# Kernel optimization log

Measured on AMD Instinct MI355X. Metric: run time of the kernel, lower is better.

The kernel has to match this reference:

```python
import jax, jax.numpy as jnp
import numpy as np

B, T, C, H = 2, 2048, 1024, 16
DH = C // H  # head_size = 64
EPS = 1e-5


def layernorm_axis1(x, gamma, beta):
    # Faithful to the torch code: mean/var over dim 1 (TIME axis), unbiased var.
    mean = jnp.mean(x, axis=1, keepdims=True)
    var = jnp.var(x, axis=1, ddof=1, keepdims=True)
    xhat = (x - mean) / jnp.sqrt(var + EPS)
    return gamma * xhat + beta


def setup_inputs() -> dict:
    key = jax.random.key(0)
    ks = jax.random.split(key, 16)
    s_in = 1.0 / np.sqrt(C)
    s_cat = 1.0 / np.sqrt(H * DH)
    s_ff = 1.0 / np.sqrt(4 * C)
    return {
        "x": jax.random.normal(ks[0], (B, T, C), dtype=jnp.float32),
        # per-head Q/K/V projections (no bias), stacked: [H, C, DH]
        "Wq": jax.random.uniform(ks[1], (H, C, DH), jnp.float32, -s_in, s_in),
        "Wk": jax.random.uniform(ks[2], (H, C, DH), jnp.float32, -s_in, s_in),
        "Wv": jax.random.uniform(ks[3], (H, C, DH), jnp.float32, -s_in, s_in),
        # attention output projection [H*DH, C] + bias
        "Wo": jax.random.uniform(ks[4], (H * DH, C), jnp.float32, -s_cat, s_cat),
        "bo": jax.random.uniform(ks[5], (C,), jnp.float32, -s_cat, s_cat),
        # FFN
        "W1": jax.random.uniform(ks[6], (C, 4 * C), jnp.float32, -s_in, s_in),
        "b1": jax.random.uniform(ks[7], (4 * C,), jnp.float32, -s_in, s_in),
        "W2": jax.random.uniform(ks[8], (4 * C, C), jnp.float32, -s_ff, s_ff),
        "b2": jax.random.uniform(ks[9], (C,), jnp.float32, -s_ff, s_ff),
        # LayerNorm affine params (plain tensors in the original)
        "gamma1": jnp.ones((C,), jnp.float32),
        "beta1": jnp.zeros((C,), jnp.float32),
        "gamma2": jnp.ones((C,), jnp.float32),
        "beta2": jnp.zeros((C,), jnp.float32),
    }


def reference(x, Wq, Wk, Wv, Wo, bo, W1, b1, W2, b2, gamma1, beta1, gamma2, beta2):
    # --- pre-LN attention sublayer ---
    x1 = layernorm_axis1(x, gamma1, beta1)                     # [B,T,C]
    q = jnp.einsum("btc,hcd->bhtd", x1, Wq)                    # [B,H,T,DH]
    k = jnp.einsum("btc,hcd->bhtd", x1, Wk)
    v = jnp.einsum("btc,hcd->bhtd", x1, Wv)
    # NOTE: scaled by full embedding dim C (not head_size) — faithful to source.
    scores = jnp.einsum("bhtd,bhsd->bhts", q, k) * (C ** -0.5)  # [B,H,T,T]
    causal = jnp.tril(jnp.ones((T, T), dtype=bool))
    scores = jnp.where(causal, scores, -jnp.inf)
    wei = jax.nn.softmax(scores, axis=-1)
    attn = jnp.einsum("bhts,bhsd->bhtd", wei, v)               # [B,H,T,DH]
    attn = attn.transpose(0, 2, 1, 3).reshape(B, T, H * DH)    # concat heads
    x = x + attn @ Wo + bo
    # --- pre-LN FFN sublayer ---
    x2 = layernorm_axis1(x, gamma2, beta2)
    h = jax.nn.relu(x2 @ W1 + b1)
    x = x + h @ W2 + b2
    return x
```

## Files before the change

### kernel.cpp

```cpp
#include <hip/hip_runtime.h>
#include <math.h>


#define TDIM 2048
#define BDIM 2
#define CDIM 1024
#define HDIM 16
#define DHE  64
#define QKVS 3072
#define NT   32
#define LNEPS 1e-5f
#define SC2  0.0450842200278f

typedef float f32x4 __attribute__((ext_vector_type(4)));
typedef __bf16 bf16x8 __attribute__((ext_vector_type(8)));
typedef __bf16 bf16x4 __attribute__((ext_vector_type(4)));

__device__ __forceinline__ void gld_lds16(const __bf16* g, __bf16* l) {
  __builtin_amdgcn_global_load_lds(
      (const __attribute__((address_space(1))) void*)g,
      (__attribute__((address_space(3))) void*)l, 16, 0, 0);
}

__global__ __launch_bounds__(256) void ln_stats(const float* __restrict__ x,
                                                float* __restrict__ sumv,
                                                float* __restrict__ sqv) {
  int c = blockIdx.x * 256 + threadIdx.x;
  int b = blockIdx.y;
  int t0 = blockIdx.z * (TDIM / 16);
  const float* xp = x + ((size_t)b * TDIM + t0) * CDIM + c;
  float s = 0.f, q = 0.f;
  for (int t = 0; t < TDIM / 16; ++t) {
    float v = xp[(size_t)t * CDIM];
    s += v;
    q += v * v;
  }
  atomicAdd(&sumv[b * CDIM + c], s);
  atomicAdd(&sqv[b * CDIM + c], q);
}

__global__ __launch_bounds__(256) void ln_apply(const float* __restrict__ x,
    const float* __restrict__ sumv, const float* __restrict__ sqv,
    const float* __restrict__ gamma, const float* __restrict__ beta,
    __bf16* __restrict__ y) {
  size_t i = (size_t)blockIdx.x * 256 + threadIdx.x;
  int c = (int)(i & (CDIM - 1));
  int b = (int)(i >> 21);
  float mean = sumv[b * CDIM + c] * (1.f / TDIM);
  float var = (sqv[b * CDIM + c] - mean * mean * (float)TDIM) * (1.f / (TDIM - 1));
  float rstd = rsqrtf(var + LNEPS);
  y[i] = (__bf16)(gamma[c] * (x[i] - mean) * rstd + beta[c]);
}

__global__ __launch_bounds__(256) void pack_all(
    const float* __restrict__ Wq, const float* __restrict__ Wk,
    const float* __restrict__ Wv, const float* __restrict__ Wo,
    const float* __restrict__ W1, const float* __restrict__ W2,
    __bf16* __restrict__ Wqkvb, __bf16* __restrict__ Wob,
    __bf16* __restrict__ W1b, __bf16* __restrict__ W2b) {
  __shared__ float tile[32][33];
  int t = blockIdx.x;
  int tx = threadIdx.x & 31, ty = threadIdx.x >> 5;
  if (t < 3072) {
    int mat = t >> 10, rem = t & 1023;
    int h = rem >> 6, rr = rem & 63;
    int c0 = (rr & 31) * 32, d0 = (rr >> 5) * 32;
    const float* W = (mat == 0) ? Wq : (mat == 1) ? Wk : Wv;
#pragma unroll
    for (int i = 0; i < 4; ++i)
      tile[ty + i * 8][tx] = W[((size_t)h * CDIM + c0 + ty + i * 8) * DHE + d0 + tx];
    __syncthreads();
#pragma unroll
    for (int i = 0; i < 4; ++i) {
      int n = mat * 1024 + h * 64 + d0 + ty + i * 8;
      Wqkvb[(size_t)n * CDIM + c0 + tx] = (__bf16)tile[tx][ty + i * 8];
    }
  } else {
    const float* in; __bf16* outp; int Cc, R, l;
    if (t < 4096)      { in = Wo; outp = Wob; R = 1024; Cc = 1024; l = t - 3072; }
    else if (t < 8192) { in = W1; outp = W1b; R = 1024; Cc = 4096; l = t - 4096; }
    else               { in = W2; outp = W2b; R = 4096; Cc = 1024; l = t - 8192; }
    int ncx = Cc >> 5;
    int c0 = (l % ncx) * 32, r0 = (l / ncx) * 32;
#pragma unroll
    for (int i = 0; i < 4; ++i)
      tile[ty + i * 8][tx] = in[(size_t)(r0 + ty + i * 8) * Cc + c0 + tx];
    __syncthreads();
#pragma unroll
    for (int i = 0; i < 4; ++i)
      outp[(size_t)(c0 + ty + i * 8) * R + r0 + tx] = (__bf16)tile[tx][ty + i * 8];
  }
}

__global__ __launch_bounds__(256) void transp_v(const __bf16* __restrict__ qkv,
    __bf16* __restrict__ vtb) {
  __shared__ __bf16 tile[32][33];
  int bh = blockIdx.y >> 1, d0 = (blockIdx.y & 1) * 32;
  int b = bh >> 4, h = bh & 15;
  int t0 = blockIdx.x * 32;
  int tx = threadIdx.x & 31, ty = threadIdx.x >> 5;
#pragma unroll
  for (int i = 0; i < 4; ++i)
    tile[ty + i * 8][tx] = qkv[((size_t)b * TDIM + t0 + ty + i * 8) * QKVS + 2048 + h * DHE + d0 + tx];
  __syncthreads();
#pragma unroll
  for (int i = 0; i < 4; ++i)
    vtb[((size_t)bh * 64 + d0 + ty + i * 8) * TDIM + t0 + tx] = tile[tx][ty + i * 8];
}

template<bool BIAS, bool RELU, bool OUTBF>
__global__ __launch_bounds__(512, 2) void gemm256(
    const __bf16* __restrict__ Ag, const __bf16* __restrict__ Bg,
    const float* __restrict__ bias, void* __restrict__ Cm, void* __restrict__ Cm2,
    int M, int N, int K, int ld, int gnx) {
  __shared__ __align__(16) char lds[131072];
  int tid = threadIdx.x;
  int lane = tid & 63, wid = tid >> 6;
  int wm = wid >> 2, wn = wid & 3;
  int l15 = lane & 15, hi = lane >> 4;

  size_t koff = (size_t)blockIdx.y * K;
  Ag += koff; Bg += koff;
  void* Cuse = blockIdx.y ? Cm2 : Cm;

  int nwg = gridDim.x;
  int q = nwg >> 3, r = nwg & 7;
  int xcd = blockIdx.x & 7, pos = blockIdx.x >> 3;
  int wgid = (xcd < r ? xcd * (q + 1) : r * (q + 1) + (xcd - r) * q) + pos;
  int m0 = (wgid / gnx) * 256, n0 = (wgid % gnx) * 256;

  int srow = tid >> 2;
  int skcol = ((tid & 3) ^ ((tid >> 3) & 3)) << 3;
  const int acS = ((hi ^ ((l15 >> 1) & 3)) << 4);

  f32x4 acc[8][4];
#pragma unroll
  for (int i = 0; i < 8; ++i)
#pragma unroll
    for (int j = 0; j < 4; ++j) acc[i][j] = (f32x4){0.f, 0.f, 0.f, 0.f};

  auto stageM = [&](const __bf16* __restrict__ G, int grow0, int k0, char* dst) {
#pragma unroll
    for (int c = 0; c < 2; ++c)
      gld_lds16(G + (size_t)(grow0 + c * 128 + srow) * ld + k0 + skcol,
                (__bf16*)(dst + c * 8192) + (size_t)tid * 8);
  };
  auto stageT = [&](int t) {
    char* dst = lds + (size_t)(t & 3) * 32768;
    stageM(Ag, m0, t << 5, dst);
    stageM(Bg, n0, t << 5, dst + 16384);
  };

  int KT = K >> 5;
  stageT(0); stageT(1); stageT(2);
  asm volatile("s_waitcnt vmcnt(8)" ::: "memory");
  __builtin_amdgcn_s_barrier();

  bf16x8 a[8], b[4];
  for (int t = 0; t < KT; ++t) {
    if (t + 3 < KT) stageT(t + 3);
    const char* buf = lds + (size_t)(t & 3) * 32768;
#pragma unroll
    for (int i = 0; i < 8; ++i)
      a[i] = *(const bf16x8*)(buf + (wm * 128 + i * 16 + l15) * 64 + acS);
#pragma unroll
    for (int j = 0; j < 4; ++j)
      b[j] = *(const bf16x8*)(buf + 16384 + (wn * 64 + j * 16 + l15) * 64 + acS);
    __builtin_amdgcn_s_setprio(1);
#pragma unroll
    for (int i = 0; i < 8; ++i)
#pragma unroll
      for (int j = 0; j < 4; ++j)
        acc[i][j] = __builtin_amdgcn_mfma_f32_16x16x32_bf16(a[i], b[j], acc[i][j], 0, 0, 0);
    __builtin_amdgcn_s_setprio(0);
    if (t + 1 < KT) {
      asm volatile("" ::: "memory");
      if (t + 3 < KT)      asm volatile("s_waitcnt vmcnt(8)" ::: "memory");
      else if (t + 2 < KT) asm volatile("s_waitcnt vmcnt(4)" ::: "memory");
      else                 asm volatile("s_waitcnt vmcnt(0)" ::: "memory");
      __builtin_amdgcn_s_barrier();
    }
  }

#pragma unroll
  for (int fm = 0; fm < 8; ++fm) {
    int row = m0 + wm * 128 + fm * 16 + hi * 4;
#pragma unroll
    for (int fn = 0; fn < 4; ++fn) {
      int col = n0 + wn * 64 + fn * 16 + l15;
#pragma unroll
      for (int j = 0; j < 4; ++j) {
        float v = acc[fm][fn][j];
        size_t off = (size_t)(row + j) * N + col;
        if (BIAS) v += bias[col];
        if (RELU) v = fmaxf(v, 0.f);
        if (OUTBF) ((__bf16*)Cuse)[off] = (__bf16)v;
        else       ((float*)Cuse)[off] = v;
      }
    }
  }
}

__global__ __launch_bounds__(256) void splitk_reduce(const float* __restrict__ p0,
    const float* __restrict__ p1, const float* __restrict__ bias,
    const float* __restrict__ res, float* __restrict__ out) {
  size_t i = ((size_t)blockIdx.x * 256 + threadIdx.x) * 4;
  int c = (int)(i & (CDIM - 1));
  float4 a = *(const float4*)(p0 + i);
  float4 b = *(const float4*)(p1 + i);
  float4 r = *(const float4*)(res + i);
  float4 bb = *(const float4*)(bias + c);
  float4 v;
  v.x = a.x + b.x + r.x + bb.x;
  v.y = a.y + b.y + r.y + bb.y;
  v.z = a.z + b.z + r.z + bb.z;
  v.w = a.w + b.w + r.w + bb.w;
  *(float4*)(out + i) = v;
}

__global__ __launch_bounds__(512, 4) void attn_mfma(const __bf16* __restrict__ qkv,
    const __bf16* __restrict__ vt, __bf16* __restrict__ o) {
  __shared__ __align__(16) char smem[55296];
  __bf16 (*Ks)[64][72] = (__bf16 (*)[64][72])(smem);
  __bf16 (*Vs)[64][72] = (__bf16 (*)[64][72])(smem + 18432);
  __bf16 (*Ps)[16][72] = (__bf16 (*)[16][72])(smem + 36864);
  float (*Os)[64]      = (float (*)[64])(smem);
  float* ms = (float*)(smem + 16384);
  float* ls = (float*)(smem + 16640);

  int bh = blockIdx.y;
  int b = bh >> 4, h = bh & 15;
  int bxA = blockIdx.x;
  int bxB = NT - 1 - bxA;
  int tid = threadIdx.x;
  int lane = tid & 63, w = tid >> 6;
  int wq = w & 3;
  int g = w >> 2;
  int l15 = lane & 15, hi = lane >> 4;
  int hi4 = hi * 4;
  size_t bT = (size_t)b * TDIM;

  bf16x8 onesb;
#pragma unroll
  for (int i = 0; i < 8; ++i) onesb[i] = (l15 == 0) ? (__bf16)1.0f : (__bf16)0.0f;

  bf16x8 qfA[2], qfB[2];
  {
    const __bf16* qp = qkv + (bT + bxA * 64 + wq * 16 + l15) * QKVS + h * DHE;
    qfA[0] = *(const bf16x8*)(qp + hi * 8);
    qfA[1] = *(const bf16x8*)(qp + 32 + hi * 8);
    qp = qkv + (bT + bxB * 64 + wq * 16 + l15) * QKVS + h * DHE;
    qfB[0] = *(const bf16x8*)(qp + hi * 8);
    qfB[1] = *(const bf16x8*)(qp + 32 + hi * 8);
  }

  float mA = -INFINITY, mB = -INFINITY;
  f32x4 lA = (f32x4){0.f, 0.f, 0.f, 0.f};
  f32x4 lB = (f32x4){0.f, 0.f, 0.f, 0.f};
  f32x4 oA[4], oB[4];
#pragma unroll
  for (int n = 0; n < 4; ++n) {
    oA[n] = (f32x4){0.f, 0.f, 0.f, 0.f};
    oB[n] = (f32x4){0.f, 0.f, 0.f, 0.f};
  }

  int g_tid = tid & 255;
  int r0 = g_tid >> 3, c8 = (g_tid & 7) * 8;

  auto process = [&](const bf16x8* qf, float& m_i, f32x4& l_acc, f32x4* oacc,
                     int bx, int t2) {
    f32x4 sacc[4];
#pragma unroll
    for (int n = 0; n < 4; ++n) sacc[n] = (f32x4){0.f, 0.f, 0.f, 0.f};
    __builtin_amdgcn_s_setprio(1);
#pragma unroll
    for (int n = 0; n < 4; ++n)
#pragma unroll
      for (int kk = 0; kk < 2; ++kk) {
        bf16x8 kf = *(const bf16x8*)&Ks[g][n * 16 + l15][kk * 32 + hi * 8];
        sacc[n] = __builtin_amdgcn_mfma_f32_16x16x32_bf16(kf, qf[kk], sacc[n], 0, 0, 0);
      }
    __builtin_amdgcn_s_setprio(0);

    int myq = wq * 16 + l15;
    if (t2 == bx) {
#pragma unroll
      for (int n = 0; n < 4; ++n)
#pragma unroll
        for (int j = 0; j < 4; ++j)
          if (n * 16 + hi4 + j > myq) sacc[n][j] = -INFINITY;
    }

    float mx = sacc[0][0];
#pragma unroll
    for (int n = 0; n < 4; ++n) {
      float a0 = fmaxf(sacc[n][0], sacc[n][1]);
      float a1 = fmaxf(sacc[n][2], sacc[n][3]);
      mx = fmaxf(mx, fmaxf(a0, a1));
    }
    mx = fmaxf(mx, __shfl_xor(mx, 16));
    mx = fmaxf(mx, __shfl_xor(mx, 32));
    mx *= SC2;

    if (!__all(mx - m_i <= 8.0f)) {
      float nm = fmaxf(m_i, mx);
      float al = exp2f(m_i - nm);
      m_i = nm;
#pragma unroll
      for (int r = 0; r < 4; ++r) {
        float ao = __shfl(al, hi4 + r);
        l_acc[r] *= ao;
#pragma unroll
        for (int n = 0; n < 4; ++n) oacc[n][r] *= ao;
      }
    }

    float negm = -m_i;
#pragma unroll
    for (int n = 0; n < 4; ++n) {
      bf16x4 pv;
#pragma unroll
      for (int j = 0; j < 4; ++j)
        pv[j] = (__bf16)exp2f(fmaf(sacc[n][j], SC2, negm));
      *(bf16x4*)&Ps[w][l15][n * 16 + hi4] = pv;
    }

    bf16x8 pa0 = *(const bf16x8*)&Ps[w][l15][hi * 8];
    bf16x8 pa1 = *(const bf16x8*)&Ps[w][l15][32 + hi * 8];
    __builtin_amdgcn_s_setprio(1);
#pragma unroll
    for (int n = 0; n < 4; ++n) {
      bf16x8 vf0 = *(const bf16x8*)&Vs[g][n * 16 + l15][hi * 8];
      bf16x8 vf1 = *(const bf16x8*)&Vs[g][n * 16 + l15][32 + hi * 8];
      oacc[n] = __builtin_amdgcn_mfma_f32_16x16x32_bf16(pa0, vf0, oacc[n], 0, 0, 0);
      oacc[n] = __builtin_amdgcn_mfma_f32_16x16x32_bf16(pa1, vf1, oacc[n], 0, 0, 0);
    }
    l_acc = __builtin_amdgcn_mfma_f32_16x16x32_bf16(pa0, onesb, l_acc, 0, 0, 0);
    l_acc = __builtin_amdgcn_mfma_f32_16x16x32_bf16(pa1, onesb, l_acc, 0, 0, 0);
    __builtin_amdgcn_s_setprio(0);
  };

  for (int j = 0; j <= bxB / 2; ++j) {
    int t2 = 2 * j + g;
    bool have = (t2 <= bxB);
    __syncthreads();
    if (have) {
#pragma unroll
      for (int rr = 0; rr < 2; ++rr) {
        int row = rr * 32 + r0;
        *(bf16x8*)&Ks[g][row][c8] =
            *(const bf16x8*)(qkv + (bT + t2 * 64 + row) * QKVS + 1024 + h * DHE + c8);
        *(bf16x8*)&Vs[g][row][c8] =
            *(const bf16x8*)(vt + ((size_t)bh * 64 + row) * TDIM + t2 * 64 + c8);
      }
    }
    __syncthreads();
    if (t2 <= bxA) process(qfA, mA, lA, oA, bxA, t2);
    if (have)      process(qfB, mB, lB, oB, bxB, t2);
  }

  auto merge = [&](int bx, float m_i, const f32x4& l_acc, f32x4* oacc) {
    float m_o[4], l_o[4];
#pragma unroll
    for (int r = 0; r < 4; ++r) {
      m_o[r] = __shfl(m_i, hi4 + r);
      l_o[r] = __shfl(l_acc[r], lane & 48);
    }
    __syncthreads();
    if (g == 1) {
#pragma unroll
      for (int r = 0; r < 4; ++r) {
        int lrow = wq * 16 + hi4 + r;
        if (l15 == 0) { ms[lrow] = m_o[r]; ls[lrow] = l_o[r]; }
#pragma unroll
        for (int n = 0; n < 4; ++n)
          Os[lrow][n * 16 + l15] = oacc[n][r];
      }
    }
    __syncthreads();
    if (g == 0) {
#pragma unroll
      for (int r = 0; r < 4; ++r) {
        int lrow = wq * 16 + hi4 + r;
        float m1 = ms[lrow], l1 = ls[lrow];
        float mm = fmaxf(m_o[r], m1);
        float e0 = exp2f(m_o[r] - mm), e1 = exp2f(m1 - mm);
        float inv = 1.f / (l_o[r] * e0 + l1 * e1);
        size_t row = bT + bx * 64 + lrow;
#pragma unroll
        for (int n = 0; n < 4; ++n) {
          float v = (oacc[n][r] * e0 + Os[lrow][n * 16 + l15] * e1) * inv;
          o[row * CDIM + h * DHE + n * 16 + l15] = (__bf16)v;
        }
      }
    }
  };
  merge(bxA, mA, lA, oA);
  merge(bxB, mB, lB, oB);
}

extern "C" void kernel_launch(void* const* d_in, const int* in_sizes, int n_in,
                              void* d_out, int out_size, void* d_ws, size_t ws_size,
                              hipStream_t stream) {
  (void)in_sizes; (void)n_in; (void)out_size; (void)ws_size;
  const float* x   = (const float*)d_in[0];
  const float* Wq  = (const float*)d_in[1];
  const float* Wk  = (const float*)d_in[2];
  const float* Wv  = (const float*)d_in[3];
  const float* Wo  = (const float*)d_in[4];
  const float* bo  = (const float*)d_in[5];
  const float* W1  = (const float*)d_in[6];
  const float* b1  = (const float*)d_in[7];
  const float* W2  = (const float*)d_in[8];
  const float* b2  = (const float*)d_in[9];
  const float* g1  = (const float*)d_in[10];
  const float* be1 = (const float*)d_in[11];
  const float* g2  = (const float*)d_in[12];
  const float* be2 = (const float*)d_in[13];
  float* out = (float*)d_out;

  char* wsb = (char*)d_ws;
  const size_t MB = 1024 * 1024;
  __bf16* Wqkvb = (__bf16*)(wsb + 0);
  __bf16* Wob   = (__bf16*)(wsb + 6  * MB);
  __bf16* W1b   = (__bf16*)(wsb + 8  * MB);
  __bf16* W2b   = (__bf16*)(wsb + 16 * MB);
  __bf16* qkvb  = (__bf16*)(wsb + 24 * MB);
  __bf16* hb    = (__bf16*)(wsb + 24 * MB);
  __bf16* vtb   = (__bf16*)(wsb + 48 * MB);
  __bf16* x1b   = (__bf16*)(wsb + 56 * MB);
  __bf16* attnb = (__bf16*)(wsb + 56 * MB);
  float*  xmid  = (float*) (wsb + 64 * MB);
  __bf16* x2b   = (__bf16*)(wsb + 80 * MB);
  float*  stats = (float*) (wsb + 88 * MB);
  float*  q0    = (float*) (wsb + 24 * MB);
  float*  q1    = (float*) (wsb + 40 * MB);
  float*  p0    = (float*) (wsb + 0);
  float*  p1    = (float*) (wsb + 48 * MB);
  float* sum1 = stats,        *sq1 = stats + 2048;
  float* sum2 = stats + 4096, *sq2 = stats + 6144;

  hipMemsetAsync(stats, 0, 4 * 2048 * sizeof(float), stream);

  pack_all<<<dim3(12288), 256, 0, stream>>>(Wq, Wk, Wv, Wo, W1, W2,
                                            Wqkvb, Wob, W1b, W2b);

  ln_stats<<<dim3(CDIM / 256, BDIM, 16), 256, 0, stream>>>(x, sum1, sq1);
  ln_apply<<<dim3((BDIM * TDIM * CDIM) / 256), 256, 0, stream>>>(x, sum1, sq1, g1, be1, x1b);

  gemm256<false, false, true><<<dim3(192, 1), 512, 0, stream>>>(
      x1b, Wqkvb, nullptr, qkvb, qkvb, 4096, 3072, 1024, 1024, 12);

  transp_v<<<dim3(TDIM / 32, 64), 256, 0, stream>>>(qkvb, vtb);

  attn_mfma<<<dim3(NT / 2, BDIM * HDIM), 512, 0, stream>>>(qkvb, vtb, attnb);

  gemm256<false, false, false><<<dim3(64, 2), 512, 0, stream>>>(
      attnb, Wob, nullptr, q0, q1, 4096, 1024, 512, 1024, 4);
  splitk_reduce<<<dim3(4096), 256, 0, stream>>>(q0, q1, bo, x, xmid);

  ln_stats<<<dim3(CDIM / 256, BDIM, 16), 256, 0, stream>>>(xmid, sum2, sq2);
  ln_apply<<<dim3((BDIM * TDIM * CDIM) / 256), 256, 0, stream>>>(xmid, sum2, sq2, g2, be2, x2b);

  gemm256<true, true, true><<<dim3(256, 1), 512, 0, stream>>>(
      x2b, W1b, b1, hb, hb, 4096, 4096, 1024, 1024, 16);

  gemm256<false, false, false><<<dim3(64, 2), 512, 0, stream>>>(
      hb, W2b, nullptr, p0, p1, 4096, 1024, 2048, 4096, 4);
  splitk_reduce<<<dim3(4096), 256, 0, stream>>>(p0, p1, b2, xmid, out);
}
```

Before: 270.1 us.

## Split GEMM k-step into two half-phases interleaving loads with MFMA

Restructures the GEMM main loop so each k-step runs as two phases. Each phase loads half of the A fragments and issues half of the global-to-LDS staging (A tile first, then B tile), separated by barriers and sched_barriers. This is meant to spread memory issue across compute, ping-pong style, and to halve the A fragment registers. In exchange it adds extra workgroup barriers per iteration, which can stall waves.

```diff
diff --git a/kernel.cpp b/kernel.cpp
--- a/kernel.cpp
+++ b/kernel.cpp
@@ -145,41 +145,60 @@
       gld_lds16(G + (size_t)(grow0 + c * 128 + srow) * ld + k0 + skcol,
                 (__bf16*)(dst + c * 8192) + (size_t)tid * 8);
   };
-  auto stageT = [&](int t) {
-    char* dst = lds + (size_t)(t & 3) * 32768;
+
+  int KT = K >> 5;
+#pragma unroll
+  for (int t = 0; t < 3; ++t) {
+    char* dst = lds + (size_t)t * 32768;
     stageM(Ag, m0, t << 5, dst);
     stageM(Bg, n0, t << 5, dst + 16384);
-  };
-
-  int KT = K >> 5;
-  stageT(0); stageT(1); stageT(2);
+  }
   asm volatile("s_waitcnt vmcnt(8)" ::: "memory");
   __builtin_amdgcn_s_barrier();
 
-  bf16x8 a[8], b[4];
+  bf16x8 a[4], b[4];
   for (int t = 0; t < KT; ++t) {
-    if (t + 3 < KT) stageT(t + 3);
     const char* buf = lds + (size_t)(t & 3) * 32768;
-#pragma unroll
-    for (int i = 0; i < 8; ++i)
+    char* bufn = lds + (size_t)((t + 3) & 3) * 32768;
+    bool st = (t + 3 < KT);
+    int k3 = (t + 3) << 5;
+
+#pragma unroll
+    for (int i = 0; i < 4; ++i)
       a[i] = *(const bf16x8*)(buf + (wm * 128 + i * 16 + l15) * 64 + acS);
 #pragma unroll
     for (int j = 0; j < 4; ++j)
       b[j] = *(const bf16x8*)(buf + 16384 + (wn * 64 + j * 16 + l15) * 64 + acS);
+    if (st) stageM(Ag, m0, k3, bufn);
+    __builtin_amdgcn_s_barrier();
+    __builtin_amdgcn_sched_barrier(0);
     __builtin_amdgcn_s_setprio(1);
 #pragma unroll
-    for (int i = 0; i < 8; ++i)
+    for (int i = 0; i < 4; ++i)
 #pragma unroll
       for (int j = 0; j < 4; ++j)
         acc[i][j] = __builtin_amdgcn_mfma_f32_16x16x32_bf16(a[i], b[j], acc[i][j], 0, 0, 0);
     __builtin_amdgcn_s_setprio(0);
-    if (t + 1 < KT) {
-      asm volatile("" ::: "memory");
-      if (t + 3 < KT)      asm volatile("s_waitcnt vmcnt(8)" ::: "memory");
-      else if (t + 2 < KT) asm volatile("s_waitcnt vmcnt(4)" ::: "memory");
-      else                 asm volatile("s_waitcnt vmcnt(0)" ::: "memory");
-      __builtin_amdgcn_s_barrier();
-    }
+    __builtin_amdgcn_s_barrier();
+
+#pragma unroll
+    for (int i = 0; i < 4; ++i)
+      a[i] = *(const bf16x8*)(buf + (wm * 128 + 64 + i * 16 + l15) * 64 + acS);
+    if (st) stageM(Bg, n0, k3, bufn + 16384);
+    __builtin_amdgcn_s_barrier();
+    __builtin_amdgcn_sched_barrier(0);
+    __builtin_amdgcn_s_setprio(1);
+#pragma unroll
+    for (int i = 0; i < 4; ++i)
+#pragma unroll
+      for (int j = 0; j < 4; ++j)
+        acc[4 + i][j] = __builtin_amdgcn_mfma_f32_16x16x32_bf16(a[i], b[j], acc[4 + i][j], 0, 0, 0);
+    __builtin_amdgcn_s_setprio(0);
+    asm volatile("" ::: "memory");
+    if (st)                  asm volatile("s_waitcnt vmcnt(8)" ::: "memory");
+    else if (t + 2 < KT)     asm volatile("s_waitcnt vmcnt(4)" ::: "memory");
+    else if (t + 1 < KT)     asm volatile("s_waitcnt vmcnt(0)" ::: "memory");
+    __builtin_amdgcn_s_barrier();
   }
 
 #pragma unroll
```

Result: slower. 276.4 us (+2.3%).

## Shrink GEMM tiles to 256x128/128x128, triple-buffer, fuse Wo reduce with LN stats

Applied to the files above, without the earlier changes.

Replaces the 256x256 GEMM with a templated kernel using 256x128 or 128x128 tiles, three LDS buffers instead of four, and higher occupancy launch bounds. The aim is more workgroups across the CUs for better wave fill. It also drops the XCD-aware workgroup remapping. The Wo split-K reduction is fused with the second LayerNorm statistics pass, saving one kernel and one read of xmid. The W2 split-K partial buffer is split across two workspace regions to fit the layout, which adds pointer-selection logic and some aliasing risk.

```diff
diff --git a/kernel.cpp b/kernel.cpp
--- a/kernel.cpp
+++ b/kernel.cpp
@@ -108,83 +108,91 @@
     vtb[((size_t)bh * 64 + d0 + ty + i * 8) * TDIM + t0 + tx] = tile[tx][ty + i * 8];
 }
 
-template<bool BIAS, bool RELU, bool OUTBF>
-__global__ __launch_bounds__(512, 2) void gemm256(
+template<int BM, bool BIAS, bool RELU, bool OUTBF>
+__global__ __launch_bounds__(BM * 2, (BM == 256) ? 4 : 3) void gemm_t(
     const __bf16* __restrict__ Ag, const __bf16* __restrict__ Bg,
-    const float* __restrict__ bias, void* __restrict__ Cm, void* __restrict__ Cm2,
+    const float* __restrict__ bias, void* __restrict__ Cm,
+    void* __restrict__ Cm2, void* __restrict__ Cm3, int msplit,
     int M, int N, int K, int ld, int gnx) {
-  __shared__ __align__(16) char lds[131072];
+  constexpr int T   = BM * 2;
+  constexpr int PB  = (BM == 256) ? 1 : 2;
+  constexpr int LPT = 2 + PB;
+  constexpr int BUF = BM * 64 + 8192;
+  __shared__ __align__(16) char lds[3 * BUF];
+
   int tid = threadIdx.x;
   int lane = tid & 63, wid = tid >> 6;
-  int wm = wid >> 2, wn = wid & 3;
+  int wm = wid >> 1, wn = wid & 1;
   int l15 = lane & 15, hi = lane >> 4;
 
   size_t koff = (size_t)blockIdx.y * K;
   Ag += koff; Bg += koff;
-  void* Cuse = blockIdx.y ? Cm2 : Cm;
-
-  int nwg = gridDim.x;
-  int q = nwg >> 3, r = nwg & 7;
-  int xcd = blockIdx.x & 7, pos = blockIdx.x >> 3;
-  int wgid = (xcd < r ? xcd * (q + 1) : r * (q + 1) + (xcd - r) * q) + pos;
-  int m0 = (wgid / gnx) * 256, n0 = (wgid % gnx) * 256;
+
+  int wgid = blockIdx.x;
+  int m0 = (wgid / gnx) * BM, n0 = (wgid % gnx) * 128;
+  void* Cuse = blockIdx.y ? (m0 < msplit ? Cm2 : Cm3) : Cm;
 
   int srow = tid >> 2;
   int skcol = ((tid & 3) ^ ((tid >> 3) & 3)) << 3;
   const int acS = ((hi ^ ((l15 >> 1) & 3)) << 4);
 
-  f32x4 acc[8][4];
-#pragma unroll
-  for (int i = 0; i < 8; ++i)
+  f32x4 acc[4][4];
+#pragma unroll
+  for (int i = 0; i < 4; ++i)
 #pragma unroll
     for (int j = 0; j < 4; ++j) acc[i][j] = (f32x4){0.f, 0.f, 0.f, 0.f};
 
-  auto stageM = [&](const __bf16* __restrict__ G, int grow0, int k0, char* dst) {
+  auto stageT = [&](int t) {
+    char* dst = lds + (size_t)(t % 3) * BUF;
+    int k0 = t << 5;
 #pragma unroll
     for (int c = 0; c < 2; ++c)
-      gld_lds16(G + (size_t)(grow0 + c * 128 + srow) * ld + k0 + skcol,
-                (__bf16*)(dst + c * 8192) + (size_t)tid * 8);
+      gld_lds16(Ag + (size_t)(m0 + c * (BM / 2) + srow) * ld + k0 + skcol,
+                (__bf16*)(dst + c * (BM * 32)) + (size_t)tid * 8);
+#pragma unroll
+    for (int c = 0; c < PB; ++c)
+      gld_lds16(Bg + (size_t)(n0 + c * (T / 4) + srow) * ld + k0 + skcol,
+                (__bf16*)(dst + BM * 64 + c * (T * 16)) + (size_t)tid * 8);
   };
-  auto stageT = [&](int t) {
-    char* dst = lds + (size_t)(t & 3) * 32768;
-    stageM(Ag, m0, t << 5, dst);
-    stageM(Bg, n0, t << 5, dst + 16384);
-  };
 
   int KT = K >> 5;
-  stageT(0); stageT(1); stageT(2);
-  asm volatile("s_waitcnt vmcnt(8)" ::: "memory");
+  stageT(0); stageT(1);
+  if constexpr (BM == 256) asm volatile("s_waitcnt vmcnt(3)" ::: "memory");
+  else                     asm volatile("s_waitcnt vmcnt(4)" ::: "memory");
   __builtin_amdgcn_s_barrier();
 
-  bf16x8 a[8], b[4];
+  bf16x8 a[4], b[4];
   for (int t = 0; t < KT; ++t) {
-    if (t + 3 < KT) stageT(t + 3);
-    const char* buf = lds + (size_t)(t & 3) * 32768;
-#pragma unroll
-    for (int i = 0; i < 8; ++i)
-      a[i] = *(const bf16x8*)(buf + (wm * 128 + i * 16 + l15) * 64 + acS);
+    if (t + 2 < KT) stageT(t + 2);
+    const char* buf = lds + (size_t)(t % 3) * BUF;
+#pragma unroll
+    for (int i = 0; i < 4; ++i)
+      a[i] = *(const bf16x8*)(buf + (wm * 64 + i * 16 + l15) * 64 + acS);
 #pragma unroll
     for (int j = 0; j < 4; ++j)
-      b[j] = *(const bf16x8*)(buf + 16384 + (wn * 64 + j * 16 + l15) * 64 + acS);
+      b[j] = *(const bf16x8*)(buf + BM * 64 + (wn * 64 + j * 16 + l15) * 64 + acS);
     __builtin_amdgcn_s_setprio(1);
 #pragma unroll
-    for (int i = 0; i < 8; ++i)
+    for (int i = 0; i < 4; ++i)
 #pragma unroll
       for (int j = 0; j < 4; ++j)
         acc[i][j] = __builtin_amdgcn_mfma_f32_16x16x32_bf16(a[i], b[j], acc[i][j], 0, 0, 0);
     __builtin_amdgcn_s_setprio(0);
     if (t + 1 < KT) {
       asm volatile("" ::: "memory");
-      if (t + 3 < KT)      asm volatile("s_waitcnt vmcnt(8)" ::: "memory");
-      else if (t + 2 < KT) asm volatile("s_waitcnt vmcnt(4)" ::: "memory");
-      else                 asm volatile("s_waitcnt vmcnt(0)" ::: "memory");
+      if (t + 2 < KT) {
+        if constexpr (BM == 256) asm volatile("s_waitcnt vmcnt(3)" ::: "memory");
+        else                     asm volatile("s_waitcnt vmcnt(4)" ::: "memory");
+      } else {
+        asm volatile("s_waitcnt vmcnt(0)" ::: "memory");
+      }
       __builtin_amdgcn_s_barrier();
     }
   }
 
 #pragma unroll
-  for (int fm = 0; fm < 8; ++fm) {
-    int row = m0 + wm * 128 + fm * 16 + hi * 4;
+  for (int fm = 0; fm < 4; ++fm) {
+    int row = m0 + wm * 64 + fm * 16 + hi * 4;
 #pragma unroll
     for (int fn = 0; fn < 4; ++fn) {
       int col = n0 + wn * 64 + fn * 16 + l15;
@@ -202,10 +210,13 @@
 }
 
 __global__ __launch_bounds__(256) void splitk_reduce(const float* __restrict__ p0,
-    const float* __restrict__ p1, const float* __restrict__ bias,
-    const float* __restrict__ res, float* __restrict__ out) {
+    const float* __restrict__ p1a, const float* __restrict__ p1b, int msplit,
+    const float* __restrict__ bias, const float* __restrict__ res,
+    float* __restrict__ out) {
   size_t i = ((size_t)blockIdx.x * 256 + threadIdx.x) * 4;
   int c = (int)(i & (CDIM - 1));
+  int row = (int)(i >> 10);
+  const float* p1 = (row < msplit) ? p1a : p1b;
   float4 a = *(const float4*)(p0 + i);
   float4 b = *(const float4*)(p1 + i);
   float4 r = *(const float4*)(res + i);
@@ -216,6 +227,27 @@
   v.z = a.z + b.z + r.z + bb.z;
   v.w = a.w + b.w + r.w + bb.w;
   *(float4*)(out + i) = v;
+}
+
+__global__ __launch_bounds__(256) void wo_reduce_ln(const float* __restrict__ q0,
+    const float* __restrict__ q1, const float* __restrict__ bo,
+    const float* __restrict__ x, float* __restrict__ xmid,
+    float* __restrict__ sumv, float* __restrict__ sqv) {
+  int c = blockIdx.x * 256 + threadIdx.x;
+  int b = blockIdx.y;
+  int t0 = blockIdx.z * (TDIM / 16);
+  size_t base = ((size_t)b * TDIM + t0) * CDIM + c;
+  float bb = bo[c];
+  float s = 0.f, q = 0.f;
+  for (int t = 0; t < TDIM / 16; ++t) {
+    size_t i = base + (size_t)t * CDIM;
+    float v = q0[i] + q1[i] + bb + x[i];
+    xmid[i] = v;
+    s += v;
+    q += v * v;
+  }
+  atomicAdd(&sumv[b * CDIM + c], s);
+  atomicAdd(&sqv[b * CDIM + c], q);
 }
 
 __global__ __launch_bounds__(512, 4) void attn_mfma(const __bf16* __restrict__ qkv,
@@ -436,7 +468,8 @@
   float*  q0    = (float*) (wsb + 24 * MB);
   float*  q1    = (float*) (wsb + 40 * MB);
   float*  p0    = (float*) (wsb + 0);
-  float*  p1    = (float*) (wsb + 48 * MB);
+  float*  p1a   = (float*) (wsb + 56 * MB);
+  float*  p1b   = (float*) (wsb + 80 * MB) - 2048 * 1024;
   float* sum1 = stats,        *sq1 = stats + 2048;
   float* sum2 = stats + 4096, *sq2 = stats + 6144;
 
@@ -448,24 +481,24 @@
   ln_stats<<<dim3(CDIM / 256, BDIM, 16), 256, 0, stream>>>(x, sum1, sq1);
   ln_apply<<<dim3((BDIM * TDIM * CDIM) / 256), 256, 0, stream>>>(x, sum1, sq1, g1, be1, x1b);
 
-  gemm256<false, false, true><<<dim3(192, 1), 512, 0, stream>>>(
-      x1b, Wqkvb, nullptr, qkvb, qkvb, 4096, 3072, 1024, 1024, 12);
+  gemm_t<256, false, false, true><<<dim3(384, 1), 512, 0, stream>>>(
+      x1b, Wqkvb, nullptr, qkvb, qkvb, qkvb, 0, 4096, 3072, 1024, 1024, 24);
 
   transp_v<<<dim3(TDIM / 32, 64), 256, 0, stream>>>(qkvb, vtb);
 
   attn_mfma<<<dim3(NT / 2, BDIM * HDIM), 512, 0, stream>>>(qkvb, vtb, attnb);
 
-  gemm256<false, false, false><<<dim3(64, 2), 512, 0, stream>>>(
-      attnb, Wob, nullptr, q0, q1, 4096, 1024, 512, 1024, 4);
-  splitk_reduce<<<dim3(4096), 256, 0, stream>>>(q0, q1, bo, x, xmid);
-
-  ln_stats<<<dim3(CDIM / 256, BDIM, 16), 256, 0, stream>>>(xmid, sum2, sq2);
+  gemm_t<128, false, false, false><<<dim3(256, 2), 256, 0, stream>>>(
+      attnb, Wob, nullptr, q0, q1, q1, 4096, 4096, 1024, 512, 1024, 8);
+  wo_reduce_ln<<<dim3(CDIM / 256, BDIM, 16), 256, 0, stream>>>(
+      q0, q1, bo, x, xmid, sum2, sq2);
+
   ln_apply<<<dim3((BDIM * TDIM * CDIM) / 256), 256, 0, stream>>>(xmid, sum2, sq2, g2, be2, x2b);
 
-  gemm256<true, true, true><<<dim3(256, 1), 512, 0, stream>>>(
-      x2b, W1b, b1, hb, hb, 4096, 4096, 1024, 1024, 16);
-
-  gemm256<false, false, false><<<dim3(64, 2), 512, 0, stream>>>(
-      hb, W2b, nullptr, p0, p1, 4096, 1024, 2048, 4096, 4);
-  splitk_reduce<<<dim3(4096), 256, 0, stream>>>(p0, p1, b2, xmid, out);
-}
+  gemm_t<256, true, true, true><<<dim3(512, 1), 512, 0, stream>>>(
+      x2b, W1b, b1, hb, hb, hb, 0, 4096, 4096, 1024, 1024, 32);
+
+  gemm_t<128, false, false, false><<<dim3(256, 2), 256, 0, stream>>>(
+      hb, W2b, nullptr, p0, p1a, p1b, 2048, 4096, 1024, 2048, 4096, 8);
+  splitk_reduce<<<dim3(4096), 256, 0, stream>>>(p0, p1a, p1b, 2048, b2, xmid, out);
+}
```

Result: faster. 260.9 us (-3.4%).
